# Optimization experiments

Hardware: AMD Instinct MI355X
Metric: run time of the kernel (lower is better)

Reference implementation:

```python
import jax, jax.numpy as jnp
import numpy as np

P_DROP = 0.1
KEEP = 1.0 - P_DROP


def setup_inputs() -> dict:
    key = jax.random.key(0)
    k1, k2, k3 = jax.random.split(key, 3)
    x1 = jax.random.normal(k1, (32, 512, 768), dtype=jnp.float32)
    x2 = jax.random.normal(k2, (32, 511, 768), dtype=jnp.float32)
    # dropout keep-mask (True = keep), Bernoulli(p_keep=0.9)
    drop_mask = jax.random.bernoulli(k3, KEEP, (32, 512, 511))
    return {"x1": x1, "x2": x2, "drop_mask": drop_mask}


def reference(x1, x2, drop_mask):
    # scores: [b, q, k] = x1 @ x2^T (scale factor is 1 in the original)
    scores = jnp.einsum("bqd,bkd->bqk", x1, x2)
    attn = jax.nn.softmax(scores, axis=-1)
    # inverted dropout with explicit mask: keep/KEEP, drop->0
    attn = jnp.where(drop_mask, attn * (1.0 / KEEP), 0.0)
    # output: [b, q, d] = attn @ x2 (x2 doubles as values)
    return jnp.einsum("bqk,bkd->bqd", attn, x2)
```

## Files before the change

### kernel.cpp

```cpp
#include <hip/hip_runtime.h>


namespace {

constexpr int NB = 32, NQ = 512, NK = 511, ND = 768;
constexpr int TQ = 64, NTH = 512;
constexpr int NCH = 24;
constexpr int NKC = 16;
constexpr float INV_KEEP = 1.0f / 0.9f;

constexpr int X1H_OFF = 0;
constexpr int X1L_OFF = 4096;
constexpr int X2H_OFF = 8192;
constexpr int X2L_OFF = 40960;
constexpr int P_OFF   = 0;
constexpr int VT_OFF  = 65536;
constexpr int RED_OFF = 114688;
constexpr int MLD_OFF = RED_OFF + 2048;
constexpr int FLD_OFF = MLD_OFF + 256;
constexpr int LDS_TOTAL = FLD_OFF + 256;

typedef short s8v  __attribute__((ext_vector_type(8)));
typedef float f32x4 __attribute__((ext_vector_type(4)));

__device__ __forceinline__ unsigned f2bf(float x) {
    unsigned u = __float_as_uint(x);
    return (u + 0x7FFFu + ((u >> 16) & 1u)) >> 16;
}
__device__ __forceinline__ unsigned pk_hi(float a, float b) {
    return f2bf(a) | (f2bf(b) << 16);
}
__device__ __forceinline__ void split2(float a, float b, unsigned& hi, unsigned& lo) {
    unsigned ha = f2bf(a), hb = f2bf(b);
    float ra = a - __uint_as_float(ha << 16);
    float rb = b - __uint_as_float(hb << 16);
    hi = ha | (hb << 16);
    lo = (__float_as_uint(ra) >> 16) | ((__float_as_uint(rb) >> 16) << 16);
}

#define SCHED0() __builtin_amdgcn_sched_barrier(0)
#define BAR()    __builtin_amdgcn_s_barrier()
#define LGKM0()  asm volatile("s_waitcnt lgkmcnt(0)" ::: "memory")

__global__ __launch_bounds__(NTH, 2)
void fused_attn(const float* __restrict__ x1, const float* __restrict__ x2,
                const int* __restrict__ dmask, float* __restrict__ out)
{
    extern __shared__ char smem[];
    const int t  = threadIdx.x;
    const int w  = t >> 6;
    const int l  = t & 63;
    const int li = l & 15;
    const int g  = l >> 4;

    const int logical = ((blockIdx.x & 7) << 5) | (blockIdx.x >> 3);
    const int b  = logical >> 3;
    const int q0 = (logical & 7) * TQ;

    const float* x1b = x1 + (size_t)(b * NQ + q0) * ND;
    const float* x2b = x2 + (size_t)b * NK * ND;
    const int*   mb  = dmask + (size_t)(b * NQ + q0) * NK;
    float*       ob  = out + (size_t)(b * NQ + q0) * ND;

    float* redp = (float*)(smem + RED_OFF);
    float* mldp = (float*)(smem + MLD_OFF);
    float* fldp = (float*)(smem + FLD_OFF);

    f32x4 acc[4][4] = {};

    f32x4 px1;
    f32x4 pxa[4], pxb[4];
    const int r0 = t >> 2, gq1 = t & 3;

    auto loadStage = [&](int dc) {
        const int d0 = dc * 32;
        px1 = *(const f32x4*)(x1b + (size_t)(t >> 3) * ND + d0 + (t & 7) * 4);
        #pragma unroll
        for (int j = 0; j < 4; ++j) {
            const int r = r0 + 128 * j;
            if (r < NK) {
                pxa[j] = *(const f32x4*)(x2b + (size_t)r * ND + d0 + gq1 * 8);
                pxb[j] = *(const f32x4*)(x2b + (size_t)r * ND + d0 + gq1 * 8 + 4);
            } else {
                pxa[j] = (f32x4){0.f, 0.f, 0.f, 0.f};
                pxb[j] = (f32x4){0.f, 0.f, 0.f, 0.f};
            }
        }
    };
    auto writeStage = [&]() {
        {
            unsigned h0, l0_, h1, l1_;
            split2(px1[0], px1[1], h0, l0_);
            split2(px1[2], px1[3], h1, l1_);
            const int q = t >> 3, cg = t & 7;
            const int a = (q >> 4) * 1024 + ((cg >> 1) * 16 + (q & 15)) * 16 + (cg & 1) * 8;
            *(uint2*)(smem + X1H_OFF + a) = make_uint2(h0, h1);
            *(uint2*)(smem + X1L_OFF + a) = make_uint2(l0_, l1_);
        }
        #pragma unroll
        for (int j = 0; j < 4; ++j) {
            const int r = r0 + 128 * j;
            unsigned hh[4], ll[4];
            split2(pxa[j][0], pxa[j][1], hh[0], ll[0]);
            split2(pxa[j][2], pxa[j][3], hh[1], ll[1]);
            split2(pxb[j][0], pxb[j][1], hh[2], ll[2]);
            split2(pxb[j][2], pxb[j][3], hh[3], ll[3]);
            const int a = (r >> 4) * 1024 + (gq1 * 16 + (r & 15)) * 16;
            *(uint4*)(smem + X2H_OFF + a) = make_uint4(hh[0], hh[1], hh[2], hh[3]);
            *(uint4*)(smem + X2L_OFF + a) = make_uint4(ll[0], ll[1], ll[2], ll[3]);
        }
    };

    loadStage(0);
    for (int dc = 0; dc < NCH; ++dc) {
        SCHED0(); BAR(); SCHED0();
        writeStage();
        if (dc + 1 < NCH) loadStage(dc + 1);
        LGKM0(); SCHED0(); BAR(); SCHED0();

        s8v ah[4], al[4], bh[4], bl[4];
        #pragma unroll
        for (int i = 0; i < 4; ++i) {
            ah[i] = *(const s8v*)(smem + X1H_OFF + i * 1024 + l * 16);
            al[i] = *(const s8v*)(smem + X1L_OFF + i * 1024 + l * 16);
            bh[i] = *(const s8v*)(smem + X2H_OFF + (w * 4 + i) * 1024 + l * 16);
            bl[i] = *(const s8v*)(smem + X2L_OFF + (w * 4 + i) * 1024 + l * 16);
        }
        #pragma unroll
        for (int qb = 0; qb < 4; ++qb)
            #pragma unroll
            for (int c = 0; c < 4; ++c) {
                acc[qb][c] = __builtin_amdgcn_mfma_f32_16x16x32_bf16(ah[qb], bh[c], acc[qb][c], 0, 0, 0);
                acc[qb][c] = __builtin_amdgcn_mfma_f32_16x16x32_bf16(ah[qb], bl[c], acc[qb][c], 0, 0, 0);
                acc[qb][c] = __builtin_amdgcn_mfma_f32_16x16x32_bf16(al[qb], bh[c], acc[qb][c], 0, 0, 0);
            }
    }
    __syncthreads();

    if (w == 7 && li == 15) {
        #pragma unroll
        for (int qb = 0; qb < 4; ++qb)
            #pragma unroll
            for (int r = 0; r < 4; ++r) acc[qb][3][r] = -3.0e38f;
    }
    #pragma unroll
    for (int qb = 0; qb < 4; ++qb)
        #pragma unroll
        for (int r = 0; r < 4; ++r) {
            float v = fmaxf(fmaxf(acc[qb][0][r], acc[qb][1][r]),
                            fmaxf(acc[qb][2][r], acc[qb][3][r]));
            v = fmaxf(v, __shfl_xor(v, 1));
            v = fmaxf(v, __shfl_xor(v, 2));
            v = fmaxf(v, __shfl_xor(v, 4));
            v = fmaxf(v, __shfl_xor(v, 8));
            if (li == 0) redp[(qb * 16 + g * 4 + r) * 8 + w] = v;
        }
    __syncthreads();
    if (t < 64) {
        float v = redp[t * 8];
        #pragma unroll
        for (int i = 1; i < 8; ++i) v = fmaxf(v, redp[t * 8 + i]);
        mldp[t] = v;
    }
    __syncthreads();
    #pragma unroll
    for (int qb = 0; qb < 4; ++qb)
        #pragma unroll
        for (int r = 0; r < 4; ++r) {
            const float m = mldp[qb * 16 + g * 4 + r];
            float e0 = __expf(acc[qb][0][r] - m);
            float e1 = __expf(acc[qb][1][r] - m);
            float e2 = __expf(acc[qb][2][r] - m);
            float e3 = __expf(acc[qb][3][r] - m);
            acc[qb][0][r] = e0; acc[qb][1][r] = e1;
            acc[qb][2][r] = e2; acc[qb][3][r] = e3;
            float s = (e0 + e1) + (e2 + e3);
            s += __shfl_xor(s, 1);
            s += __shfl_xor(s, 2);
            s += __shfl_xor(s, 4);
            s += __shfl_xor(s, 8);
            if (li == 0) redp[(qb * 16 + g * 4 + r) * 8 + w] = s;
        }
    __syncthreads();
    if (t < 64) {
        float s = redp[t * 8];
        #pragma unroll
        for (int i = 1; i < 8; ++i) s += redp[t * 8 + i];
        fldp[t] = INV_KEEP / s;
    }
    #pragma unroll
    for (int qb = 0; qb < 4; ++qb)
        #pragma unroll
        for (int c = 0; c < 4; ++c)
            #pragma unroll
            for (int r = 0; r < 4; ++r) {
                const int q = qb * 16 + g * 4 + r;
                const int k = w * 64 + c * 16 + li;
                float p = 0.f;
                if (k < NK && mb[(size_t)q * NK + k] != 0) p = acc[qb][c][r];
                float po = __shfl_xor(p, 1);
                if ((li & 1) == 0)
                    *(unsigned*)(smem + P_OFF + qb * 16384 + (k >> 5) * 1024 +
                                 ((k >> 3) & 3) * 256 + (q & 15) * 16 + (k & 7) * 2) = pk_hi(p, po);
            }

    f32x4 o[4][6] = {};
    f32x4 va[8], vb[8];
    const int dqA = t >> 2, gqA = t & 3;
    const int dqB = 128 + (t >> 2);

    auto loadV = [&](int kc) {
        const int kbase = kc * 32;
        #pragma unroll
        for (int e = 0; e < 8; ++e) {
            const int k = kbase + gqA * 8 + e;
            va[e] = (k < NK) ? *(const f32x4*)(x2b + (size_t)k * ND + dqA * 4)
                             : (f32x4){0.f, 0.f, 0.f, 0.f};
        }
        if (t < 256) {
            #pragma unroll
            for (int e = 0; e < 8; ++e) {
                const int k = kbase + gqA * 8 + e;
                vb[e] = (k < NK) ? *(const f32x4*)(x2b + (size_t)k * ND + dqB * 4)
                                 : (f32x4){0.f, 0.f, 0.f, 0.f};
            }
        }
    };
    auto writeV = [&]() {
        #pragma unroll
        for (int c = 0; c < 4; ++c) {
            const int d = dqA * 4 + c;
            const int wp = d / 96, rem = d - wp * 96;
            const int a = VT_OFF + (wp * 6 + (rem >> 4)) * 1024 + gqA * 256 + ((d & 15) ^ gqA) * 16;
            *(uint4*)(smem + a) = make_uint4(pk_hi(va[0][c], va[1][c]), pk_hi(va[2][c], va[3][c]),
                                             pk_hi(va[4][c], va[5][c]), pk_hi(va[6][c], va[7][c]));
        }
        if (t < 256) {
            #pragma unroll
            for (int c = 0; c < 4; ++c) {
                const int d = dqB * 4 + c;
                const int wp = d / 96, rem = d - wp * 96;
                const int a = VT_OFF + (wp * 6 + (rem >> 4)) * 1024 + gqA * 256 + ((d & 15) ^ gqA) * 16;
                *(uint4*)(smem + a) = make_uint4(pk_hi(vb[0][c], vb[1][c]), pk_hi(vb[2][c], vb[3][c]),
                                                 pk_hi(vb[4][c], vb[5][c]), pk_hi(vb[6][c], vb[7][c]));
            }
        }
    };

    loadV(0);
    __syncthreads();
    for (int kc = 0; kc < NKC; ++kc) {
        SCHED0(); BAR(); SCHED0();
        writeV();
        if (kc + 1 < NKC) loadV(kc + 1);
        LGKM0(); SCHED0(); BAR(); SCHED0();

        s8v pa[4], pb[6];
        #pragma unroll
        for (int qb = 0; qb < 4; ++qb)
            pa[qb] = *(const s8v*)(smem + P_OFF + qb * 16384 + kc * 1024 + l * 16);
        #pragma unroll
        for (int nf = 0; nf < 6; ++nf)
            pb[nf] = *(const s8v*)(smem + VT_OFF + (w * 6 + nf) * 1024 + g * 256 + (li ^ g) * 16);
        #pragma unroll
        for (int qb = 0; qb < 4; ++qb)
            #pragma unroll
            for (int nf = 0; nf < 6; ++nf)
                o[qb][nf] = __builtin_amdgcn_mfma_f32_16x16x32_bf16(pa[qb], pb[nf], o[qb][nf], 0, 0, 0);
    }

    #pragma unroll
    for (int qb = 0; qb < 4; ++qb)
        #pragma unroll
        for (int r = 0; r < 4; ++r) {
            const float f = fldp[qb * 16 + g * 4 + r];
            #pragma unroll
            for (int nf = 0; nf < 6; ++nf)
                ob[(size_t)(qb * 16 + g * 4 + r) * ND + w * 96 + nf * 16 + li] = o[qb][nf][r] * f;
        }
}

}

extern "C" void kernel_launch(void* const* d_in, const int* in_sizes, int n_in,
                              void* d_out, int out_size, void* d_ws, size_t ws_size,
                              hipStream_t stream)
{
    const float* x1    = (const float*)d_in[0];
    const float* x2    = (const float*)d_in[1];
    const int*   dmask = (const int*)d_in[2];
    float*       out   = (float*)d_out;

    (void)hipFuncSetAttribute((const void*)fused_attn,
                              hipFuncAttributeMaxDynamicSharedMemorySize, LDS_TOTAL);
    fused_attn<<<dim3(NB * (NQ / TQ)), dim3(NTH), LDS_TOTAL, stream>>>(x1, x2, dmask, out);
}
```

Measured before the change: 286.4 us.

## Double-buffer LDS stages in both GEMM loops with one barrier per iteration

Measured after the change: 278.5 us. -2.8%, faster.

```diff
diff --git a/kernel.cpp b/kernel.cpp
--- a/kernel.cpp
+++ b/kernel.cpp
@@ -9,18 +9,21 @@
 constexpr int NKC = 16;
 constexpr float INV_KEEP = 1.0f / 0.9f;
 
-constexpr int X1H_OFF = 0;
-constexpr int X1L_OFF = 4096;
-constexpr int X2H_OFF = 8192;
-constexpr int X2L_OFF = 40960;
-constexpr int P_OFF   = 0;
-constexpr int VT_OFF  = 65536;
-constexpr int RED_OFF = 114688;
+constexpr int BUF0   = 0;
+constexpr int BUF1   = 73728;
+constexpr int X1H_O  = 0;
+constexpr int X1L_O  = 4096;
+constexpr int X2H_O  = 8192;
+constexpr int X2L_O  = 40960;
+constexpr int P_OFF  = 0;
+constexpr int VT0    = 65536;
+constexpr int VT1    = 114688;
+constexpr int RED_OFF = 150528;
 constexpr int MLD_OFF = RED_OFF + 2048;
 constexpr int FLD_OFF = MLD_OFF + 256;
-constexpr int LDS_TOTAL = FLD_OFF + 256;
-
-typedef short s8v  __attribute__((ext_vector_type(8)));
+constexpr int LDS_TOTAL = 163840;
+
+typedef short s8v   __attribute__((ext_vector_type(8)));
 typedef float f32x4 __attribute__((ext_vector_type(4)));
 
 __device__ __forceinline__ unsigned f2bf(float x) {
@@ -37,10 +40,6 @@
     hi = ha | (hb << 16);
     lo = (__float_as_uint(ra) >> 16) | ((__float_as_uint(rb) >> 16) << 16);
 }
-
-#define SCHED0() __builtin_amdgcn_sched_barrier(0)
-#define BAR()    __builtin_amdgcn_s_barrier()
-#define LGKM0()  asm volatile("s_waitcnt lgkmcnt(0)" ::: "memory")
 
 __global__ __launch_bounds__(NTH, 2)
 void fused_attn(const float* __restrict__ x1, const float* __restrict__ x2,
@@ -87,15 +86,15 @@
             }
         }
     };
-    auto writeStage = [&]() {
+    auto writeStage = [&](char* bb) {
         {
             unsigned h0, l0_, h1, l1_;
             split2(px1[0], px1[1], h0, l0_);
             split2(px1[2], px1[3], h1, l1_);
             const int q = t >> 3, cg = t & 7;
             const int a = (q >> 4) * 1024 + ((cg >> 1) * 16 + (q & 15)) * 16 + (cg & 1) * 8;
-            *(uint2*)(smem + X1H_OFF + a) = make_uint2(h0, h1);
-            *(uint2*)(smem + X1L_OFF + a) = make_uint2(l0_, l1_);
+            *(uint2*)(bb + X1H_O + a) = make_uint2(h0, h1);
+            *(uint2*)(bb + X1L_O + a) = make_uint2(l0_, l1_);
         }
         #pragma unroll
         for (int j = 0; j < 4; ++j) {
@@ -106,25 +105,29 @@
             split2(pxb[j][0], pxb[j][1], hh[2], ll[2]);
             split2(pxb[j][2], pxb[j][3], hh[3], ll[3]);
             const int a = (r >> 4) * 1024 + (gq1 * 16 + (r & 15)) * 16;
-            *(uint4*)(smem + X2H_OFF + a) = make_uint4(hh[0], hh[1], hh[2], hh[3]);
-            *(uint4*)(smem + X2L_OFF + a) = make_uint4(ll[0], ll[1], ll[2], ll[3]);
+            *(uint4*)(bb + X2H_O + a) = make_uint4(hh[0], hh[1], hh[2], hh[3]);
+            *(uint4*)(bb + X2L_O + a) = make_uint4(ll[0], ll[1], ll[2], ll[3]);
         }
     };
 
     loadStage(0);
+    writeStage(smem + BUF0);
+    loadStage(1);
+    __syncthreads();
+
     for (int dc = 0; dc < NCH; ++dc) {
-        SCHED0(); BAR(); SCHED0();
-        writeStage();
-        if (dc + 1 < NCH) loadStage(dc + 1);
-        LGKM0(); SCHED0(); BAR(); SCHED0();
+        char* cb = smem + ((dc & 1) ? BUF1 : BUF0);
+        char* nb = smem + ((dc & 1) ? BUF0 : BUF1);
+        if (dc + 1 < NCH) writeStage(nb);
+        if (dc + 2 < NCH) loadStage(dc + 2);
 
         s8v ah[4], al[4], bh[4], bl[4];
         #pragma unroll
         for (int i = 0; i < 4; ++i) {
-            ah[i] = *(const s8v*)(smem + X1H_OFF + i * 1024 + l * 16);
-            al[i] = *(const s8v*)(smem + X1L_OFF + i * 1024 + l * 16);
-            bh[i] = *(const s8v*)(smem + X2H_OFF + (w * 4 + i) * 1024 + l * 16);
-            bl[i] = *(const s8v*)(smem + X2L_OFF + (w * 4 + i) * 1024 + l * 16);
+            ah[i] = *(const s8v*)(cb + X1H_O + i * 1024 + l * 16);
+            al[i] = *(const s8v*)(cb + X1L_O + i * 1024 + l * 16);
+            bh[i] = *(const s8v*)(cb + X2H_O + (w * 4 + i) * 1024 + l * 16);
+            bl[i] = *(const s8v*)(cb + X2L_O + (w * 4 + i) * 1024 + l * 16);
         }
         #pragma unroll
         for (int qb = 0; qb < 4; ++qb)
@@ -134,8 +137,8 @@
                 acc[qb][c] = __builtin_amdgcn_mfma_f32_16x16x32_bf16(ah[qb], bl[c], acc[qb][c], 0, 0, 0);
                 acc[qb][c] = __builtin_amdgcn_mfma_f32_16x16x32_bf16(al[qb], bh[c], acc[qb][c], 0, 0, 0);
             }
-    }
-    __syncthreads();
+        __syncthreads();
+    }
 
     if (w == 7 && li == 15) {
         #pragma unroll
@@ -188,6 +191,14 @@
         for (int i = 1; i < 8; ++i) s += redp[t * 8 + i];
         fldp[t] = INV_KEEP / s;
     }
+    __syncthreads();
+
+    float fr[4][4];
+    #pragma unroll
+    for (int qb = 0; qb < 4; ++qb)
+        #pragma unroll
+        for (int r = 0; r < 4; ++r) fr[qb][r] = fldp[qb * 16 + g * 4 + r];
+
     #pragma unroll
     for (int qb = 0; qb < 4; ++qb)
         #pragma unroll
@@ -226,34 +237,37 @@
             }
         }
     };
-    auto writeV = [&]() {
+    auto writeV = [&](char* vbase) {
         #pragma unroll
         for (int c = 0; c < 4; ++c) {
             const int d = dqA * 4 + c;
             const int wp = d / 96, rem = d - wp * 96;
-            const int a = VT_OFF + (wp * 6 + (rem >> 4)) * 1024 + gqA * 256 + ((d & 15) ^ gqA) * 16;
-            *(uint4*)(smem + a) = make_uint4(pk_hi(va[0][c], va[1][c]), pk_hi(va[2][c], va[3][c]),
-                                             pk_hi(va[4][c], va[5][c]), pk_hi(va[6][c], va[7][c]));
+            const int a = (wp * 6 + (rem >> 4)) * 1024 + gqA * 256 + ((d & 15) ^ gqA) * 16;
+            *(uint4*)(vbase + a) = make_uint4(pk_hi(va[0][c], va[1][c]), pk_hi(va[2][c], va[3][c]),
+                                              pk_hi(va[4][c], va[5][c]), pk_hi(va[6][c], va[7][c]));
         }
         if (t < 256) {
             #pragma unroll
             for (int c = 0; c < 4; ++c) {
                 const int d = dqB * 4 + c;
                 const int wp = d / 96, rem = d - wp * 96;
-                const int a = VT_OFF + (wp * 6 + (rem >> 4)) * 1024 + gqA * 256 + ((d & 15) ^ gqA) * 16;
-                *(uint4*)(smem + a) = make_uint4(pk_hi(vb[0][c], vb[1][c]), pk_hi(vb[2][c], vb[3][c]),
-                                                 pk_hi(vb[4][c], vb[5][c]), pk_hi(vb[6][c], vb[7][c]));
+                const int a = (wp * 6 + (rem >> 4)) * 1024 + gqA * 256 + ((d & 15) ^ gqA) * 16;
+                *(uint4*)(vbase + a) = make_uint4(pk_hi(vb[0][c], vb[1][c]), pk_hi(vb[2][c], vb[3][c]),
+                                                  pk_hi(vb[4][c], vb[5][c]), pk_hi(vb[6][c], vb[7][c]));
             }
         }
     };
 
     loadV(0);
-    __syncthreads();
+    writeV(smem + VT0);
+    loadV(1);
+    __syncthreads();
+
     for (int kc = 0; kc < NKC; ++kc) {
-        SCHED0(); BAR(); SCHED0();
-        writeV();
-        if (kc + 1 < NKC) loadV(kc + 1);
-        LGKM0(); SCHED0(); BAR(); SCHED0();
+        char* cv = smem + ((kc & 1) ? VT1 : VT0);
+        char* nv = smem + ((kc & 1) ? VT0 : VT1);
+        if (kc + 1 < NKC) writeV(nv);
+        if (kc + 2 < NKC) loadV(kc + 2);
 
         s8v pa[4], pb[6];
         #pragma unroll
@@ -261,19 +275,20 @@
             pa[qb] = *(const s8v*)(smem + P_OFF + qb * 16384 + kc * 1024 + l * 16);
         #pragma unroll
         for (int nf = 0; nf < 6; ++nf)
-            pb[nf] = *(const s8v*)(smem + VT_OFF + (w * 6 + nf) * 1024 + g * 256 + (li ^ g) * 16);
+            pb[nf] = *(const s8v*)(cv + (w * 6 + nf) * 1024 + g * 256 + (li ^ g) * 16);
         #pragma unroll
         for (int qb = 0; qb < 4; ++qb)
             #pragma unroll
             for (int nf = 0; nf < 6; ++nf)
                 o[qb][nf] = __builtin_amdgcn_mfma_f32_16x16x32_bf16(pa[qb], pb[nf], o[qb][nf], 0, 0, 0);
+        __syncthreads();
     }
 
     #pragma unroll
     for (int qb = 0; qb < 4; ++qb)
         #pragma unroll
         for (int r = 0; r < 4; ++r) {
-            const float f = fldp[qb * 16 + g * 4 + r];
+            const float f = fr[qb][r];
             #pragma unroll
             for (int nf = 0; nf < 6; ++nf)
                 ob[(size_t)(qb * 16 + g * 4 + r) * ND + w * 96 + nf * 16 + li] = o[qb][nf][r] * f;
```
